# Performance work log

Measured on AMD Instinct MI355X. Metric: run time of the kernel, lower is better.

The kernel has to match this reference:

```python
import jax, jax.numpy as jnp
import numpy as np

N_NODES = 32768
EMB_DIM = 128
N_CODES = 4096
N_GRAPHS = 512
ALPHA = 0.5            # args.alpha_init buffer
COMMIT_W = 1.0         # args.commitment_weight
BN_EPS = 1e-5


def setup_inputs() -> dict:
    key = jax.random.key(0)
    ks = jax.random.split(key, 8)
    node_feat = jax.random.normal(ks[0], (N_NODES, EMB_DIM), dtype=jnp.float32)
    score = jax.random.uniform(ks[1], (N_NODES, 1), dtype=jnp.float32)
    batch = jnp.sort(jax.random.randint(ks[2], (N_NODES,), 0, N_GRAPHS)).astype(jnp.int64)
    codebook_c = jax.random.normal(ks[3], (N_CODES, EMB_DIM), dtype=jnp.float32)
    codebook_s = jax.random.normal(ks[4], (N_CODES, EMB_DIM), dtype=jnp.float32)
    w1 = jax.random.normal(ks[5], (EMB_DIM, 2 * EMB_DIM), dtype=jnp.float32) * (1.0 / np.sqrt(EMB_DIM))
    b1 = jnp.zeros((2 * EMB_DIM,), dtype=jnp.float32)
    gamma = jnp.ones((2 * EMB_DIM,), dtype=jnp.float32)
    beta = jnp.zeros((2 * EMB_DIM,), dtype=jnp.float32)
    run_mean = jnp.zeros((2 * EMB_DIM,), dtype=jnp.float32)
    run_var = jnp.ones((2 * EMB_DIM,), dtype=jnp.float32)
    w2 = jax.random.normal(ks[6], (2 * EMB_DIM, 1), dtype=jnp.float32) * (1.0 / np.sqrt(2 * EMB_DIM))
    b2 = jnp.zeros((1,), dtype=jnp.float32)
    return {"node_feat": node_feat, "score": score, "batch": batch,
            "codebook_c": codebook_c, "codebook_s": codebook_s,
            "w1": w1, "b1": b1, "gamma": gamma, "beta": beta,
            "run_mean": run_mean, "run_var": run_var, "w2": w2, "b2": b2}


def _vector_quantize(x, codebook):
    # squared euclidean distance [N, K]; argmin lookup with straight-through.
    d2 = (jnp.sum(x * x, axis=-1, keepdims=True)
          - 2.0 * (x @ codebook.T)
          + jnp.sum(codebook * codebook, axis=-1))
    idx = jnp.argmin(d2, axis=-1)                     # [N]
    quantize = codebook[idx]                          # gather [N, D]
    commit_loss = jnp.mean((jax.lax.stop_gradient(quantize) - x) ** 2) * COMMIT_W
    out = x + jax.lax.stop_gradient(quantize - x)     # straight-through estimator
    return out, idx, commit_loss


def _mean_pool(x, batch):
    sums = jax.ops.segment_sum(x, batch, num_segments=N_GRAPHS)
    counts = jax.ops.segment_sum(jnp.ones((x.shape[0], 1), x.dtype), batch, num_segments=N_GRAPHS)
    return sums / jnp.maximum(counts, 1.0)


def reference(node_feat, score, batch, codebook_c, codebook_s,
              w1, b1, gamma, beta, run_mean, run_var, w2, b2):
    h_c = node_feat * score + ALPHA * node_feat * (1.0 - score)
    h_s = node_feat * (1.0 - score) + ALPHA * node_feat * score
    vq_c, _, cmt_loss_c = _vector_quantize(h_c, codebook_c)
    vq_s, _, cmt_loss_s = _vector_quantize(h_s, codebook_s)
    c_node_feat = node_feat * score + vq_c
    s_node_feat = node_feat * (1.0 - score) + vq_s
    c_graph_feat = _mean_pool(c_node_feat, batch)
    s_graph_feat = _mean_pool(s_node_feat, batch)
    # classifier: Linear -> BatchNorm1d (eval) -> ReLU -> Dropout(identity) -> Linear
    h = c_graph_feat @ w1 + b1
    h = (h - run_mean) * jax.lax.rsqrt(run_var + BN_EPS) * gamma + beta
    h = jax.nn.relu(h)
    c_logit = h @ w2 + b2
    return (c_logit, c_graph_feat, s_graph_feat, cmt_loss_c, cmt_loss_s, c_node_feat, s_node_feat)
```

## Files before the change

kernel.cpp:

```cpp
#include <hip/hip_runtime.h>
#include <hip/hip_bf16.h>

#define NODES   32768
#define DIM     128
#define NCODES  4096
#define NGRAPHS 512
#define THR     0.0625f

#define OFF_LOGIT 0
#define OFF_CG    512
#define OFF_SG    66048
#define OFF_LC    131584
#define OFF_LS    131585
#define OFF_CN    131586
#define OFF_SN    4325890

#define SPLIT_U16   263680
#define PLANE_U16   524288
#define HALF_F32    1180416
#define CSLOT_F32   1442560

#define WS_CNORM    0
#define WS_IDX      32768
#define WS_FLAGCNT  294928
#define WS_STARTS   294936
#define WS_FLAGLIST 296988
#define FLAG_CAP    32767

typedef __attribute__((ext_vector_type(8))) _Float16 f16x8_t;
typedef __attribute__((ext_vector_type(4))) float f32x4_t;

__device__ __forceinline__ float h_of(float x, float sc, int cb) {
    float omsc = __fsub_rn(1.0f, sc);
    float half_x = __fmul_rn(0.5f, x);
    if (cb == 0)
        return __fadd_rn(__fmul_rn(x, sc), __fmul_rn(half_x, omsc));
    else
        return __fadd_rn(__fmul_rn(x, omsc), __fmul_rn(half_x, sc));
}

__device__ __forceinline__ unsigned short f2h(float f) {
    return __builtin_bit_cast(unsigned short, (_Float16)f);
}

__device__ __forceinline__ void gload_lds16(const void* g, void* l) {
    __builtin_amdgcn_global_load_lds(
        (const __attribute__((address_space(1))) int*)g,
        (__attribute__((address_space(3))) int*)l, 16, 0, 0);
}

__device__ __forceinline__ unsigned sortkey(float f) {
    unsigned b = __float_as_uint(f);
    return (b & 0x80000000u) ? ~b : (b | 0x80000000u);
}
__device__ __forceinline__ float keyinv(unsigned k) {
    unsigned b = (k & 0x80000000u) ? (k & 0x7FFFFFFFu) : ~k;
    return __uint_as_float(b);
}

__global__ __launch_bounds__(256) void prep_kernel(
    const float* __restrict__ cb_c, const float* __restrict__ cb_s,
    const int* __restrict__ batch,
    float* __restrict__ cnorm, unsigned short* __restrict__ splits,
    int* __restrict__ starts, int* __restrict__ flagcnt)
{
    int gwave = (blockIdx.x * 256 + threadIdx.x) >> 6;
    int lane  = threadIdx.x & 63;

    if (gwave < 2 * NCODES) {
        int cb = gwave >> 12, row = gwave & (NCODES - 1);
        const float* cp = (cb ? cb_s : cb_c) + (size_t)row * DIM;
        float2 v = ((const float2*)cp)[lane];
        float p = __fadd_rn(__fmul_rn(v.x, v.x), __fmul_rn(v.y, v.y));
        #pragma unroll
        for (int off = 32; off; off >>= 1) p = __fadd_rn(p, __shfl_xor(p, off, 64));
        if (lane == 0) cnorm[cb * NCODES + row] = p;
        unsigned int* hp = (unsigned int*)(splits + (size_t)cb * PLANE_U16);
        hp[row * 64 + lane] = (unsigned)f2h(v.x) | ((unsigned)f2h(v.y) << 16);
    } else {
        int w1 = gwave - 2 * NCODES;
        int g = w1 * 64 + lane;
        if (g <= NGRAPHS) {
            int lo = 0, hi = NODES;
            while (lo < hi) { int mid = (lo + hi) >> 1; if (batch[mid] < g) lo = mid + 1; else hi = mid; }
            starts[g] = lo;
        }
        if (w1 == 0 && lane < 2) flagcnt[lane] = 0;
    }
}

__global__ __launch_bounds__(256, 4) void vq_main_kernel(
    const float* __restrict__ node_feat, const float* __restrict__ score,
    const unsigned short* __restrict__ splits, const float* __restrict__ cnorm,
    unsigned long long* __restrict__ halfres)
{
    __shared__ unsigned short lds[16384];
    const int nb    = blockIdx.x & 255;
    const int half  = blockIdx.x >> 8;
    const int cb    = blockIdx.y;
    const int nbase = nb * 128;
    const int tid = threadIdx.x;
    const int w   = tid >> 6;
    const int l15 = tid & 15;
    const int lg  = (tid & 63) >> 4;
    const int swz = (tid & 7) << 4;
    const float* cnp = cnorm + cb * NCODES + half * 2048;

    #pragma unroll
    for (int i = 0; i < 16; ++i) {
        int idx = i * 1024 + tid * 4;
        int row = idx >> 7, k = idx & 127;
        float4 x = *(const float4*)&node_feat[(size_t)(nbase + row) * DIM + k];
        float sc = score[nbase + row];
        unsigned u0 = f2h(h_of(x.x, sc, cb)), u1 = f2h(h_of(x.y, sc, cb));
        unsigned u2 = f2h(h_of(x.z, sc, cb)), u3 = f2h(h_of(x.w, sc, cb));
        int abyte = row * 256 + ((2 * k) ^ ((row & 7) << 4));
        uint2 hw; hw.x = u0 | (u1 << 16); hw.y = u2 | (u3 << 16);
        *(uint2*)((char*)lds + abyte) = hw;
    }
    __syncthreads();

    f16x8_t ahi[2][4];
    int colbyte[4];
    #pragma unroll
    for (int ch = 0; ch < 4; ++ch) colbyte[ch] = (ch * 64 + lg * 16) ^ swz;
    #pragma unroll
    for (int rs = 0; rs < 2; ++rs)
        #pragma unroll
        for (int ch = 0; ch < 4; ++ch) {
            int row = 32 * w + 16 * rs + l15;
            ahi[rs][ch] = *(const f16x8_t*)((const char*)lds + row * 256 + colbyte[ch]);
        }
    __syncthreads();

    const unsigned short* wplane = splits + (size_t)cb * PLANE_U16 + half * 262144;
    int soff[4];
    #pragma unroll
    for (int i = 0; i < 4; ++i) {
        int row = w * 16 + i * 4 + lg;
        soff[i] = row * 256 + ((l15 * 16) ^ ((row & 7) << 4));
    }

    {
        const char* tb = (const char*)wplane;
        #pragma unroll
        for (int i = 0; i < 4; ++i)
            gload_lds16(tb + soff[i], (char*)lds + w * 4096 + i * 1024);
    }
    __syncthreads();

    const float NEG_INF = -3.4e38f;
    float b1v[2][4], b2v[2][4]; int b1i[2][4];
    #pragma unroll
    for (int rs = 0; rs < 2; ++rs)
        #pragma unroll
        for (int r = 0; r < 4; ++r) { b1v[rs][r] = NEG_INF; b2v[rs][r] = NEG_INF; b1i[rs][r] = 0; }

    for (int t = 0; t < 32; ++t) {
        int bs_cur = (t & 1) << 14;
        float cnc[4];
        #pragma unroll
        for (int cs = 0; cs < 4; ++cs) cnc[cs] = cnp[t * 64 + cs * 16 + l15];
        if (t < 31) {
            int bs_nxt = ((t + 1) & 1) << 14;
            const char* tb = (const char*)wplane + (t + 1) * 16384;
            #pragma unroll
            for (int i = 0; i < 4; ++i)
                gload_lds16(tb + soff[i], (char*)lds + bs_nxt + w * 4096 + i * 1024);
        }

        #pragma unroll
        for (int cp = 0; cp < 2; ++cp) {
            f32x4_t acc[2][2];
            #pragma unroll
            for (int rs = 0; rs < 2; ++rs)
                #pragma unroll
                for (int c2 = 0; c2 < 2; ++c2) acc[rs][c2] = (f32x4_t){0.f, 0.f, 0.f, 0.f};

            #pragma unroll
            for (int ch = 0; ch < 4; ++ch)
                #pragma unroll
                for (int c2 = 0; c2 < 2; ++c2) {
                    int cs = cp * 2 + c2;
                    f16x8_t bh = *(const f16x8_t*)((const char*)lds + bs_cur +
                                                   (cs * 16 + l15) * 256 + colbyte[ch]);
                    acc[0][c2] = __builtin_amdgcn_mfma_f32_16x16x32_f16(ahi[0][ch], bh, acc[0][c2], 0, 0, 0);
                    acc[1][c2] = __builtin_amdgcn_mfma_f32_16x16x32_f16(ahi[1][ch], bh, acc[1][c2], 0, 0, 0);
                }

            #pragma unroll
            for (int c2 = 0; c2 < 2; ++c2) {
                int cs = cp * 2 + c2;
                int code = half * 2048 + t * 64 + cs * 16 + l15;
                #pragma unroll
                for (int rs = 0; rs < 2; ++rs)
                    #pragma unroll
                    for (int r = 0; r < 4; ++r) {
                        float a = __fmaf_rn(-0.5f, cnc[cs], acc[rs][c2][r]);
                        bool gt = a > b1v[rs][r];
                        float nb2 = __builtin_amdgcn_fmed3f(a, b1v[rs][r], b2v[rs][r]);
                        if (gt) b1i[rs][r] = code;
                        b1v[rs][r] = fmaxf(a, b1v[rs][r]);
                        b2v[rs][r] = nb2;
                    }
            }
        }
        __syncthreads();
    }

    #pragma unroll
    for (int off = 1; off < 16; off <<= 1) {
        #pragma unroll
        for (int rs = 0; rs < 2; ++rs)
            #pragma unroll
            for (int r = 0; r < 4; ++r) {
                float ov1 = __shfl_xor(b1v[rs][r], off, 64);
                int   oi  = __shfl_xor(b1i[rs][r], off, 64);
                float ov2 = __shfl_xor(b2v[rs][r], off, 64);
                bool take = (ov1 > b1v[rs][r]) || (ov1 == b1v[rs][r] && oi < b1i[rs][r]);
                float loser = fminf(ov1, b1v[rs][r]);
                b1v[rs][r] = fmaxf(ov1, b1v[rs][r]);
                if (take) b1i[rs][r] = oi;
                b2v[rs][r] = fmaxf(loser, fmaxf(ov2, b2v[rs][r]));
            }
    }
    if (l15 == 0) {
        #pragma unroll
        for (int rs = 0; rs < 2; ++rs)
            #pragma unroll
            for (int r = 0; r < 4; ++r) {
                int node = nbase + 32 * w + 16 * rs + 4 * lg + r;
                unsigned key = sortkey(b1v[rs][r]);
                unsigned pay = (unsigned)b1i[rs][r] |
                               ((b1v[rs][r] - b2v[rs][r] < THR) ? 0x1000u : 0u);
                halfres[((size_t)(cb * 2 + half)) * NODES + node] =
                    ((unsigned long long)key << 32) | pay;
            }
    }
}

__global__ __launch_bounds__(256) void resolve_kernel(
    const unsigned long long* __restrict__ hr, unsigned long long* __restrict__ cslot,
    int* __restrict__ idx_ws, int* __restrict__ flagcnt, int* __restrict__ flaglist)
{
    int cb = blockIdx.y;
    int node = blockIdx.x * 256 + threadIdx.x;
    unsigned long long A = hr[((size_t)(cb * 2 + 0)) * NODES + node];
    unsigned long long B = hr[((size_t)(cb * 2 + 1)) * NODES + node];
    unsigned ka = (unsigned)(A >> 32), kb = (unsigned)(B >> 32);
    bool awin = ka >= kb;
    unsigned long long W = awin ? A : B;
    float aw = keyinv(awin ? ka : kb);
    float al = keyinv(awin ? kb : ka);
    bool flag = ((W >> 12) & 1ull) || (__fsub_rn(aw, al) < THR);
    idx_ws[cb * NODES + node] = (int)(W & 0xFFFu);
    if (flag) cslot[(size_t)cb * NODES + node] = ~0ull;

    unsigned long long mask = __ballot(flag);
    if (mask) {
        int lane = threadIdx.x & 63;
        int leader = __ffsll((long long)mask) - 1;
        int base = 0;
        if (lane == leader) base = atomicAdd(flagcnt + cb, (int)__popcll(mask));
        base = __shfl(base, leader, 64);
        if (flag) {
            int pos = base + (int)__popcll(mask & ((1ull << lane) - 1ull));
            if (pos < FLAG_CAP) flaglist[cb * FLAG_CAP + pos] = node;
        }
    }
}

__global__ __launch_bounds__(256) void vq_cleanup_kernel(
    const float* __restrict__ node_feat, const float* __restrict__ score,
    const float* __restrict__ cb_c, const float* __restrict__ cb_s,
    const float* __restrict__ cnorm, const int* __restrict__ flagcnt,
    const int* __restrict__ flaglist, unsigned long long* __restrict__ slots)
{
    __shared__ float cbT[128][65];
    __shared__ float hbuf[4][128];
    const int cb  = blockIdx.y;
    const int seg = blockIdx.x & 63;
    const int ng  = blockIdx.x >> 6;
    const float* cbp = cb ? cb_s : cb_c;
    const int* list = flaglist + cb * FLAG_CAP;
    int cnt = flagcnt[cb]; if (cnt > FLAG_CAP) cnt = FLAG_CAP;
    const int tid = threadIdx.x, w = tid >> 6, l = tid & 63;

    {
        int c = tid >> 2, ks = (tid & 3) * 32;
        const float* src = cbp + (size_t)(seg * 64 + c) * DIM + ks;
        #pragma unroll
        for (int j = 0; j < 8; ++j) {
            float4 v = *(const float4*)(src + j * 4);
            cbT[ks + j * 4 + 0][c] = v.x;
            cbT[ks + j * 4 + 1][c] = v.y;
            cbT[ks + j * 4 + 2][c] = v.z;
            cbT[ks + j * 4 + 3][c] = v.w;
        }
    }
    const int mycode = seg * 64 + l;
    const float cn = cnorm[cb * NCODES + mycode];
    __syncthreads();

    for (int base = ng * 4; base < cnt; base += 64) {
        int e = base + w;
        bool valid = e < cnt;
        int node = list[valid ? e : 0];
        float sc = score[node];
        float x0 = node_feat[(size_t)node * DIM + l];
        float x1 = node_feat[(size_t)node * DIM + 64 + l];
        float h0 = h_of(x0, sc, cb), h1 = h_of(x1, sc, cb);
        hbuf[w][l] = h0; hbuf[w][64 + l] = h1;
        float sxx = __fadd_rn(__fmul_rn(h0, h0), __fmul_rn(h1, h1));
        #pragma unroll
        for (int off = 32; off; off >>= 1) sxx = __fadd_rn(sxx, __shfl_xor(sxx, off, 64));
        asm volatile("s_waitcnt lgkmcnt(0)" ::: "memory");

        float p0 = 0.f, p1 = 0.f, p2 = 0.f, p3 = 0.f;
        #pragma unroll 8
        for (int m = 0; m < 32; ++m) {
            p0 = fmaf(hbuf[w][4 * m + 0], cbT[4 * m + 0][l], p0);
            p1 = fmaf(hbuf[w][4 * m + 1], cbT[4 * m + 1][l], p1);
            p2 = fmaf(hbuf[w][4 * m + 2], cbT[4 * m + 2][l], p2);
            p3 = fmaf(hbuf[w][4 * m + 3], cbT[4 * m + 3][l], p3);
        }
        float dot = __fadd_rn(__fadd_rn(p0, p1), __fadd_rn(p2, p3));
        float d2 = __fadd_rn(__fsub_rn(sxx, __fmul_rn(2.0f, dot)), cn);

        unsigned b = __float_as_uint(d2);
        unsigned key = (b & 0x80000000u) ? ~b : (b | 0x80000000u);
        unsigned long long pk = ((unsigned long long)key << 32) | (unsigned)mycode;
        #pragma unroll
        for (int off = 1; off < 64; off <<= 1) {
            unsigned long long o = __shfl_xor(pk, off, 64);
            pk = (o < pk) ? o : pk;
        }
        if (valid && l == 0)
            atomicMin(&slots[(size_t)cb * NODES + node], pk);
        asm volatile("s_waitcnt lgkmcnt(0)" ::: "memory");
    }
}

__global__ __launch_bounds__(256) void flag_writeback_kernel(
    const int* __restrict__ flagcnt, const int* __restrict__ flaglist,
    const unsigned long long* __restrict__ slots, int* __restrict__ idx_ws)
{
    int gt = blockIdx.x * 256 + threadIdx.x;
    int c0 = flagcnt[0]; if (c0 > FLAG_CAP) c0 = FLAG_CAP;
    int c1 = flagcnt[1]; if (c1 > FLAG_CAP) c1 = FLAG_CAP;
    for (int e = gt; e < 2 * FLAG_CAP; e += 256 * 256) {
        int cb = (e >= FLAG_CAP) ? 1 : 0;
        int i = e - cb * FLAG_CAP;
        int cnt = cb ? c1 : c0;
        if (i < cnt) {
            int node = flaglist[cb * FLAG_CAP + i];
            idx_ws[cb * NODES + node] =
                (int)(slots[(size_t)cb * NODES + node] & 0xFFFFFFFFull);
        }
    }
}

__global__ __launch_bounds__(256) void gather_kernel(
    const float* __restrict__ node_feat, const float* __restrict__ score,
    const float* __restrict__ cb_c, const float* __restrict__ cb_s,
    const int* __restrict__ idx_all, float* __restrict__ out,
    double* __restrict__ partials)
{
    __shared__ float redc[4], reds[4];
    int wave = threadIdx.x >> 6, lane = threadIdx.x & 63;
    int node = blockIdx.x * 4 + wave;
    float sc = score[node];
    float2 x  = *(const float2*)&node_feat[(size_t)node * DIM + 2 * lane];
    int ic = idx_all[node], is_ = idx_all[NODES + node];
    float2 qc = *(const float2*)&cb_c[(size_t)ic * DIM + 2 * lane];
    float2 qs = *(const float2*)&cb_s[(size_t)is_ * DIM + 2 * lane];

    float omsc = __fsub_rn(1.0f, sc);
    float2 cn, sn;
    cn.x = __fadd_rn(__fmul_rn(x.x, sc), qc.x);
    cn.y = __fadd_rn(__fmul_rn(x.y, sc), qc.y);
    sn.x = __fadd_rn(__fmul_rn(x.x, omsc), qs.x);
    sn.y = __fadd_rn(__fmul_rn(x.y, omsc), qs.y);
    *(float2*)&out[OFF_CN + (size_t)node * DIM + 2 * lane] = cn;
    *(float2*)&out[OFF_SN + (size_t)node * DIM + 2 * lane] = sn;

    float hc1 = h_of(x.x, sc, 0), hc2 = h_of(x.y, sc, 0);
    float hs1 = h_of(x.x, sc, 1), hs2 = h_of(x.y, sc, 1);
    float d1 = qc.x - hc1, d2 = qc.y - hc2;
    float e1 = qs.x - hs1, e2 = qs.y - hs2;
    float lc = d1 * d1 + d2 * d2;
    float ls = e1 * e1 + e2 * e2;
    #pragma unroll
    for (int off = 32; off; off >>= 1) {
        lc += __shfl_down(lc, off, 64);
        ls += __shfl_down(ls, off, 64);
    }
    if (lane == 0) { redc[wave] = lc; reds[wave] = ls; }
    __syncthreads();
    if (threadIdx.x == 0) {
        partials[blockIdx.x]        = (double)redc[0] + redc[1] + redc[2] + redc[3];
        partials[8192 + blockIdx.x] = (double)reds[0] + reds[1] + reds[2] + reds[3];
    }
}

__global__ __launch_bounds__(256) void loss_reduce_kernel(
    const double* __restrict__ partials, float* __restrict__ out)
{
    __shared__ double red[4];
    int b = blockIdx.x, t = threadIdx.x, w = t >> 6, l = t & 63;
    const double* p = partials + b * 8192;
    double s = 0.0;
    #pragma unroll 4
    for (int i = t; i < 8192; i += 256) s += p[i];
    #pragma unroll
    for (int off = 32; off; off >>= 1) s += __shfl_down(s, off, 64);
    if (l == 0) red[w] = s;
    __syncthreads();
    if (t == 0) {
        double tot = (red[0] + red[1]) + (red[2] + red[3]);
        out[OFF_LC + b] = (float)(tot * (1.0 / 4194304.0));
    }
}

__global__ __launch_bounds__(256) void pool_kernel(
    const int* __restrict__ starts, float* __restrict__ out)
{
    int g = blockIdx.x;
    int half = threadIdx.x >> 7, d = threadIdx.x & 127;
    int s = starts[g], e = starts[g + 1];
    const float* src = out + (half ? OFF_SN : OFF_CN);
    float sum = 0.0f;
    for (int n = s; n < e; ++n) sum = __fadd_rn(sum, src[(size_t)n * DIM + d]);
    float cnt = fmaxf((float)(e - s), 1.0f);
    out[(half ? OFF_SG : OFF_CG) + g * DIM + d] = __fdiv_rn(sum, cnt);
}

__global__ __launch_bounds__(256) void classifier_kernel(
    const float* __restrict__ w1, const float* __restrict__ b1,
    const float* __restrict__ gamma, const float* __restrict__ beta,
    const float* __restrict__ rm, const float* __restrict__ rv,
    const float* __restrict__ w2, const float* __restrict__ b2,
    float* __restrict__ out)
{
    __shared__ float row[DIM];
    __shared__ float red[4];
    int g = blockIdx.x, t = threadIdx.x;
    if (t < DIM) row[t] = out[OFF_CG + g * DIM + t];
    __syncthreads();
    float h = 0.0f;
    #pragma unroll 8
    for (int k = 0; k < DIM; ++k) h = fmaf(row[k], w1[k * 256 + t], h);
    h = __fadd_rn(h, b1[t]);
    float inv = __frsqrt_rn(__fadd_rn(rv[t], 1e-5f));
    h = __fadd_rn(__fmul_rn(__fmul_rn(__fsub_rn(h, rm[t]), inv), gamma[t]), beta[t]);
    h = fmaxf(h, 0.0f);
    float p = __fmul_rn(h, w2[t]);
    #pragma unroll
    for (int off = 32; off; off >>= 1) p += __shfl_down(p, off, 64);
    if ((t & 63) == 0) red[t >> 6] = p;
    __syncthreads();
    if (t == 0) {
        float total = __fadd_rn(__fadd_rn(red[0], red[1]), __fadd_rn(red[2], red[3]));
        out[OFF_LOGIT + g] = __fadd_rn(total, b2[0]);
    }
}

extern "C" void kernel_launch(void* const* d_in, const int* in_sizes, int n_in,
                              void* d_out, int out_size, void* d_ws, size_t ws_size,
                              hipStream_t stream) {
    const float* node_feat = (const float*)d_in[0];
    const float* score     = (const float*)d_in[1];
    const int*   batch     = (const int*)d_in[2];
    const float* cb_c      = (const float*)d_in[3];
    const float* cb_s      = (const float*)d_in[4];
    const float* w1        = (const float*)d_in[5];
    const float* b1        = (const float*)d_in[6];
    const float* gamma     = (const float*)d_in[7];
    const float* beta      = (const float*)d_in[8];
    const float* rm        = (const float*)d_in[9];
    const float* rv        = (const float*)d_in[10];
    const float* w2        = (const float*)d_in[11];
    const float* b2        = (const float*)d_in[12];
    float* out = (float*)d_out;
    char*  ws  = (char*)d_ws;

    float*  cnorm    = (float*)(ws + WS_CNORM);
    int*    idx      = (int*)(ws + WS_IDX);
    int*    flagcnt  = (int*)(ws + WS_FLAGCNT);
    int*    starts   = (int*)(ws + WS_STARTS);
    int*    flaglist = (int*)(ws + WS_FLAGLIST);
    unsigned short* splits = (unsigned short*)d_out + SPLIT_U16;
    unsigned long long* halfres = (unsigned long long*)(out + HALF_F32);
    unsigned long long* cslot   = (unsigned long long*)(out + CSLOT_F32);
    double* partials = (double*)(out + OFF_CG);

    prep_kernel<<<2051, 256, 0, stream>>>(cb_c, cb_s, batch, cnorm, splits,
                                          starts, flagcnt);
    vq_main_kernel<<<dim3(512, 2), 256, 0, stream>>>(node_feat, score, splits, cnorm,
                                                     halfres);
    resolve_kernel<<<dim3(128, 2), 256, 0, stream>>>(halfres, cslot, idx,
                                                     flagcnt, flaglist);
    vq_cleanup_kernel<<<dim3(1024, 2), 256, 0, stream>>>(node_feat, score, cb_c, cb_s,
                                                         cnorm, flagcnt, flaglist, cslot);
    flag_writeback_kernel<<<256, 256, 0, stream>>>(flagcnt, flaglist, cslot, idx);
    gather_kernel<<<8192, 256, 0, stream>>>(node_feat, score, cb_c, cb_s, idx, out, partials);
    loss_reduce_kernel<<<2, 256, 0, stream>>>(partials, out);
    pool_kernel<<<512, 256, 0, stream>>>(starts, out);
    classifier_kernel<<<512, 256, 0, stream>>>(w1, b1, gamma, beta, rm, rv, w2, b2, out);
}
```

Before: 350.3 us.

## Fold code-norm bias into MFMA accumulator init and batch two nodes per wave in cleanup

In the main VQ kernel, the -0.5*||c||^2 term is now preloaded into the MFMA accumulators, which drops the per-element FMA from the argmin epilogue. The cleanup kernel replaces the transposed padded codebook tile with a row-major XOR-swizzled layout that can be read as float4, and each wave now processes two flagged nodes per iteration so each codebook load is reused twice. This is meant to cut LDS traffic and epilogue ALU work, at the cost of more registers and a larger LDS footprint. Accumulating the bias first can change rounding slightly.

Measured after the change: 338.7 us. 3.3% less time.

```diff
diff --git a/kernel.cpp b/kernel.cpp
--- a/kernel.cpp
+++ b/kernel.cpp
@@ -160,7 +160,7 @@
         int bs_cur = (t & 1) << 14;
         float cnc[4];
         #pragma unroll
-        for (int cs = 0; cs < 4; ++cs) cnc[cs] = cnp[t * 64 + cs * 16 + l15];
+        for (int cs = 0; cs < 4; ++cs) cnc[cs] = __fmul_rn(-0.5f, cnp[t * 64 + cs * 16 + l15]);
         if (t < 31) {
             int bs_nxt = ((t + 1) & 1) << 14;
             const char* tb = (const char*)wplane + (t + 1) * 16384;
@@ -175,7 +175,10 @@
             #pragma unroll
             for (int rs = 0; rs < 2; ++rs)
                 #pragma unroll
-                for (int c2 = 0; c2 < 2; ++c2) acc[rs][c2] = (f32x4_t){0.f, 0.f, 0.f, 0.f};
+                for (int c2 = 0; c2 < 2; ++c2) {
+                    float iv = cnc[cp * 2 + c2];
+                    acc[rs][c2] = (f32x4_t){iv, iv, iv, iv};
+                }
 
             #pragma unroll
             for (int ch = 0; ch < 4; ++ch)
@@ -196,7 +199,7 @@
                 for (int rs = 0; rs < 2; ++rs)
                     #pragma unroll
                     for (int r = 0; r < 4; ++r) {
-                        float a = __fmaf_rn(-0.5f, cnc[cs], acc[rs][c2][r]);
+                        float a = acc[rs][c2][r];
                         bool gt = a > b1v[rs][r];
                         float nb2 = __builtin_amdgcn_fmed3f(a, b1v[rs][r], b2v[rs][r]);
                         if (gt) b1i[rs][r] = code;
@@ -276,8 +279,8 @@
     const float* __restrict__ cnorm, const int* __restrict__ flagcnt,
     const int* __restrict__ flaglist, unsigned long long* __restrict__ slots)
 {
-    __shared__ float cbT[128][65];
-    __shared__ float hbuf[4][128];
+    __shared__ char cbS[32768];
+    __shared__ float hbuf[8][128];
     const int cb  = blockIdx.y;
     const int seg = blockIdx.x & 63;
     const int ng  = blockIdx.x >> 6;
@@ -289,54 +292,69 @@
     {
         int c = tid >> 2, ks = (tid & 3) * 32;
         const float* src = cbp + (size_t)(seg * 64 + c) * DIM + ks;
+        char* dst = cbS + c * 512;
+        int sw = (c & 7) << 4;
         #pragma unroll
         for (int j = 0; j < 8; ++j) {
             float4 v = *(const float4*)(src + j * 4);
-            cbT[ks + j * 4 + 0][c] = v.x;
-            cbT[ks + j * 4 + 1][c] = v.y;
-            cbT[ks + j * 4 + 2][c] = v.z;
-            cbT[ks + j * 4 + 3][c] = v.w;
+            *(float4*)(dst + ((ks * 4 + j * 16) ^ sw)) = v;
         }
     }
     const int mycode = seg * 64 + l;
     const float cn = cnorm[cb * NCODES + mycode];
-    __syncthreads();
-
-    for (int base = ng * 4; base < cnt; base += 64) {
-        int e = base + w;
-        bool valid = e < cnt;
-        int node = list[valid ? e : 0];
-        float sc = score[node];
-        float x0 = node_feat[(size_t)node * DIM + l];
-        float x1 = node_feat[(size_t)node * DIM + 64 + l];
-        float h0 = h_of(x0, sc, cb), h1 = h_of(x1, sc, cb);
-        hbuf[w][l] = h0; hbuf[w][64 + l] = h1;
-        float sxx = __fadd_rn(__fmul_rn(h0, h0), __fmul_rn(h1, h1));
-        #pragma unroll
-        for (int off = 32; off; off >>= 1) sxx = __fadd_rn(sxx, __shfl_xor(sxx, off, 64));
+    const int swl = (l & 7) << 4;
+    const char* crow = cbS + l * 512;
+    __syncthreads();
+
+    for (int base = ng * 8; base < cnt; base += 128) {
+        int eA = base + 2 * w, eB = eA + 1;
+        bool vA = eA < cnt, vB = eB < cnt;
+        int nA = list[vA ? eA : 0], nB = list[vB ? eB : 0];
+        float scA = score[nA], scB = score[nB];
+        float a0 = h_of(node_feat[(size_t)nA * DIM + l],      scA, cb);
+        float a1 = h_of(node_feat[(size_t)nA * DIM + 64 + l], scA, cb);
+        float b0 = h_of(node_feat[(size_t)nB * DIM + l],      scB, cb);
+        float b1 = h_of(node_feat[(size_t)nB * DIM + 64 + l], scB, cb);
+        hbuf[2 * w][l] = a0;     hbuf[2 * w][64 + l] = a1;
+        hbuf[2 * w + 1][l] = b0; hbuf[2 * w + 1][64 + l] = b1;
+        float sxA = __fadd_rn(__fmul_rn(a0, a0), __fmul_rn(a1, a1));
+        float sxB = __fadd_rn(__fmul_rn(b0, b0), __fmul_rn(b1, b1));
+        #pragma unroll
+        for (int off = 32; off; off >>= 1) {
+            sxA = __fadd_rn(sxA, __shfl_xor(sxA, off, 64));
+            sxB = __fadd_rn(sxB, __shfl_xor(sxB, off, 64));
+        }
         asm volatile("s_waitcnt lgkmcnt(0)" ::: "memory");
 
-        float p0 = 0.f, p1 = 0.f, p2 = 0.f, p3 = 0.f;
+        float pA0 = 0.f, pA1 = 0.f, pA2 = 0.f, pA3 = 0.f;
+        float pB0 = 0.f, pB1 = 0.f, pB2 = 0.f, pB3 = 0.f;
+        const float4* hA = (const float4*)hbuf[2 * w];
+        const float4* hB = (const float4*)hbuf[2 * w + 1];
         #pragma unroll 8
         for (int m = 0; m < 32; ++m) {
-            p0 = fmaf(hbuf[w][4 * m + 0], cbT[4 * m + 0][l], p0);
-            p1 = fmaf(hbuf[w][4 * m + 1], cbT[4 * m + 1][l], p1);
-            p2 = fmaf(hbuf[w][4 * m + 2], cbT[4 * m + 2][l], p2);
-            p3 = fmaf(hbuf[w][4 * m + 3], cbT[4 * m + 3][l], p3);
-        }
-        float dot = __fadd_rn(__fadd_rn(p0, p1), __fadd_rn(p2, p3));
-        float d2 = __fadd_rn(__fsub_rn(sxx, __fmul_rn(2.0f, dot)), cn);
-
-        unsigned b = __float_as_uint(d2);
-        unsigned key = (b & 0x80000000u) ? ~b : (b | 0x80000000u);
-        unsigned long long pk = ((unsigned long long)key << 32) | (unsigned)mycode;
+            float4 c4 = *(const float4*)(crow + ((m * 16) ^ swl));
+            float4 ha = hA[m], hb = hB[m];
+            pA0 = fmaf(ha.x, c4.x, pA0); pA1 = fmaf(ha.y, c4.y, pA1);
+            pA2 = fmaf(ha.z, c4.z, pA2); pA3 = fmaf(ha.w, c4.w, pA3);
+            pB0 = fmaf(hb.x, c4.x, pB0); pB1 = fmaf(hb.y, c4.y, pB1);
+            pB2 = fmaf(hb.z, c4.z, pB2); pB3 = fmaf(hb.w, c4.w, pB3);
+        }
+        float dotA = __fadd_rn(__fadd_rn(pA0, pA1), __fadd_rn(pA2, pA3));
+        float dotB = __fadd_rn(__fadd_rn(pB0, pB1), __fadd_rn(pB2, pB3));
+        float dA = __fadd_rn(__fsub_rn(sxA, __fmul_rn(2.0f, dotA)), cn);
+        float dB = __fadd_rn(__fsub_rn(sxB, __fmul_rn(2.0f, dotB)), cn);
+
+        unsigned long long pkA = ((unsigned long long)sortkey(dA) << 32) | (unsigned)mycode;
+        unsigned long long pkB = ((unsigned long long)sortkey(dB) << 32) | (unsigned)mycode;
         #pragma unroll
         for (int off = 1; off < 64; off <<= 1) {
-            unsigned long long o = __shfl_xor(pk, off, 64);
-            pk = (o < pk) ? o : pk;
-        }
-        if (valid && l == 0)
-            atomicMin(&slots[(size_t)cb * NODES + node], pk);
+            unsigned long long oA = __shfl_xor(pkA, off, 64);
+            unsigned long long oB = __shfl_xor(pkB, off, 64);
+            pkA = (oA < pkA) ? oA : pkA;
+            pkB = (oB < pkB) ? oB : pkB;
+        }
+        if (l == 0 && vA) atomicMin(&slots[(size_t)cb * NODES + nA], pkA);
+        if (l == 0 && vB) atomicMin(&slots[(size_t)cb * NODES + nB], pkB);
         asm volatile("s_waitcnt lgkmcnt(0)" ::: "memory");
     }
 }
```
